# Kernel tuning notes

Hardware: AMD Instinct MI355X
Metric: run time of the kernel (lower is better)

The kernel has to match this reference:

```python
import jax, jax.numpy as jnp
import numpy as np

B, S, D = 2, 2048, 2048
H = 32
HD = D // H  # 64


def setup_inputs() -> dict:
    key = jax.random.key(0)
    ks = jax.random.split(key, 7)
    s = 1.0 / np.sqrt(D)
    return {
        "hidden_states": jax.random.normal(ks[0], (B, S, D), dtype=jnp.float32),
        "Wq": jax.random.normal(ks[1], (D, D), dtype=jnp.float32) * s,
        "Wk": jax.random.normal(ks[2], (D, D), dtype=jnp.float32) * s,
        "Wv": jax.random.normal(ks[3], (D, D), dtype=jnp.float32) * s,
        "Wf": jax.random.normal(ks[4], (H, D), dtype=jnp.float32) * s,
        "bf": jax.random.normal(ks[5], (H,), dtype=jnp.float32) * 0.1,
        "Wo": jax.random.normal(ks[6], (D, D), dtype=jnp.float32) * s,
    }


def _forgetting_attn(x, Wq, Wk, Wv, Wf, bf, Wo):
    b, s, _ = x.shape
    # projections (torch Linear: y = x @ W.T)
    q = (x @ Wq.T).reshape(b, s, H, HD)
    k = (x @ Wk.T).reshape(b, s, H, HD)
    v = (x @ Wv.T).reshape(b, s, H, HD)
    # per-head log-sigmoid forget gates, fp32, cumulative sum over time
    f = jax.nn.log_sigmoid((x @ Wf.T + bf).astype(jnp.float32))  # [b, s, H]
    c = jnp.cumsum(f, axis=1)  # [b, s, H]
    scale = 1.0 / np.sqrt(HD)
    # scores with forget bias: c_i - c_j
    scores = jnp.einsum("bihd,bjhd->bhij", q, k) * scale
    scores = scores + (c[:, :, None, :] - c[:, None, :, :]).transpose(0, 3, 1, 2)
    causal = jnp.tril(jnp.ones((s, s), dtype=bool))
    scores = jnp.where(causal[None, None], scores, -jnp.inf)
    p = jax.nn.softmax(scores, axis=-1)
    o = jnp.einsum("bhij,bjhd->bihd", p, v).reshape(b, s, D)
    return o @ Wo.T


def reference(hidden_states, Wq, Wk, Wv, Wf, bf, Wo):
    return _forgetting_attn(hidden_states, Wq, Wk, Wv, Wf, bf, Wo)
```

## Files before the change

kernel.cpp:

```cpp
#include <hip/hip_runtime.h>
#include <math.h>

#define B 2
#define S 2048
#define D 2048
#define H 32
#define HD 64
#define M (B*S)

typedef short s16x8 __attribute__((ext_vector_type(8)));
typedef float f32x4 __attribute__((ext_vector_type(4)));

__device__ __forceinline__ unsigned short f2bf(float f) {
    unsigned u = __float_as_uint(f);
    return (unsigned short)((u + 0x7fffu + ((u >> 16) & 1u)) >> 16);
}
__device__ __forceinline__ float bf2f(unsigned short h) {
    return __uint_as_float(((unsigned)h) << 16);
}

__global__ __launch_bounds__(256) void split_kernel(
    const float* __restrict__ in, unsigned short* __restrict__ hi,
    unsigned short* __restrict__ lo, int n)
{
    const int idx = (blockIdx.x * 256 + threadIdx.x) * 8;
    if (idx >= n) return;
    float f[8];
    *(float4*)&f[0] = *(const float4*)(in + idx);
    *(float4*)&f[4] = *(const float4*)(in + idx + 4);
    unsigned short h[8], l[8];
    #pragma unroll
    for (int e = 0; e < 8; ++e) {
        h[e] = f2bf(f[e]);
        l[e] = f2bf(f[e] - bf2f(h[e]));
    }
    *(s16x8*)&hi[idx] = *(s16x8*)&h[0];
    *(s16x8*)&lo[idx] = *(s16x8*)&l[0];
}

#define GBM 128
#define GBN 128
#define GBK 32
#define GLD (GBK + 8)

__global__ __launch_bounds__(256) void gemm_pre(
    const unsigned short* __restrict__ Agh, const unsigned short* __restrict__ Agl,
    const unsigned short* __restrict__ Bgh, const unsigned short* __restrict__ Bgl,
    float* __restrict__ Cf, unsigned short* __restrict__ Ch,
    unsigned short* __restrict__ Cl, int Ndim, int Kdim)
{
    __shared__ unsigned short Ah[GBM * GLD], Al[GBM * GLD];
    __shared__ unsigned short Bh[GBN * GLD], Bl[GBN * GLD];
    const int tid = threadIdx.x;
    const int nwg = gridDim.x, cpx = nwg >> 3;
    const int wg = (blockIdx.x & 7) * cpx + (blockIdx.x >> 3);
    const int ntn = Ndim / GBN;
    const int m0 = (wg / ntn) * GBM, n0 = (wg % ntn) * GBN;

    const int row = tid >> 1;
    const int seg = (tid & 1) << 4;
    const size_t abase = (size_t)(m0 + row) * Kdim + seg;
    const size_t bbase = (size_t)(n0 + row) * Kdim + seg;
    const int sbase = row * GLD + seg;

    const int wv = tid >> 6, lane = tid & 63;
    const int wr = (wv >> 1) << 6, wc = (wv & 1) << 6;
    const int fr = lane & 15, ko = (lane >> 4) << 3;

    f32x4 acc[4][4] = {};
    for (int k0 = 0; k0 < Kdim; k0 += GBK) {
        *(s16x8*)&Ah[sbase]     = *(const s16x8*)&Agh[abase + k0];
        *(s16x8*)&Ah[sbase + 8] = *(const s16x8*)&Agh[abase + k0 + 8];
        *(s16x8*)&Al[sbase]     = *(const s16x8*)&Agl[abase + k0];
        *(s16x8*)&Al[sbase + 8] = *(const s16x8*)&Agl[abase + k0 + 8];
        *(s16x8*)&Bh[sbase]     = *(const s16x8*)&Bgh[bbase + k0];
        *(s16x8*)&Bh[sbase + 8] = *(const s16x8*)&Bgh[bbase + k0 + 8];
        *(s16x8*)&Bl[sbase]     = *(const s16x8*)&Bgl[bbase + k0];
        *(s16x8*)&Bl[sbase + 8] = *(const s16x8*)&Bgl[bbase + k0 + 8];
        __syncthreads();
        s16x8 fah[4], fal[4], fbh[4], fbl[4];
        #pragma unroll
        for (int m = 0; m < 4; ++m) {
            const int r = (wr + m * 16 + fr) * GLD + ko;
            fah[m] = *(s16x8*)&Ah[r];
            fal[m] = *(s16x8*)&Al[r];
        }
        #pragma unroll
        for (int n = 0; n < 4; ++n) {
            const int r = (wc + n * 16 + fr) * GLD + ko;
            fbh[n] = *(s16x8*)&Bh[r];
            fbl[n] = *(s16x8*)&Bl[r];
        }
        #pragma unroll
        for (int m = 0; m < 4; ++m)
            #pragma unroll
            for (int n = 0; n < 4; ++n) {
                acc[m][n] = __builtin_amdgcn_mfma_f32_16x16x32_bf16(fah[m], fbh[n], acc[m][n], 0, 0, 0);
                acc[m][n] = __builtin_amdgcn_mfma_f32_16x16x32_bf16(fah[m], fbl[n], acc[m][n], 0, 0, 0);
                acc[m][n] = __builtin_amdgcn_mfma_f32_16x16x32_bf16(fal[m], fbh[n], acc[m][n], 0, 0, 0);
            }
        __syncthreads();
    }
    const int crow0 = m0 + wr + ((lane >> 4) << 2);
    const int ccol0 = n0 + wc + fr;
    #pragma unroll
    for (int m = 0; m < 4; ++m)
        #pragma unroll
        for (int n = 0; n < 4; ++n)
            #pragma unroll
            for (int r = 0; r < 4; ++r) {
                const float c = acc[m][n][r];
                const size_t idx = (size_t)(crow0 + m * 16 + r) * Ndim + ccol0 + n * 16;
                if (Cf) Cf[idx] = c;
                if (Ch) {
                    const unsigned short hh = f2bf(c);
                    Ch[idx] = hh;
                    if (Cl) Cl[idx] = f2bf(c - bf2f(hh));
                }
            }
}

__global__ __launch_bounds__(256) void fgate_kernel(
    const float* __restrict__ x, const float* __restrict__ Wf,
    const float* __restrict__ bfv, float* __restrict__ F)
{
    __shared__ float xs[D];
    const int bs = blockIdx.x;
    const float* xr = x + (size_t)bs * D;
    for (int i = threadIdx.x * 4; i < D; i += 256 * 4)
        *(float4*)&xs[i] = *(const float4*)&xr[i];
    __syncthreads();
    const int wave = threadIdx.x >> 6, lane = threadIdx.x & 63;
    for (int h = wave * 8; h < wave * 8 + 8; ++h) {
        const float* wr = Wf + (size_t)h * D;
        float sum = 0.f;
        for (int i = lane * 4; i < D; i += 64 * 4) {
            float4 w4 = *(const float4*)&wr[i];
            sum += xs[i]*w4.x + xs[i+1]*w4.y + xs[i+2]*w4.z + xs[i+3]*w4.w;
        }
        #pragma unroll
        for (int off = 32; off > 0; off >>= 1) sum += __shfl_down(sum, off);
        if (lane == 0) {
            float z = sum + bfv[h];
            F[(size_t)bs * H + h] = fminf(z, 0.f) - log1pf(expf(-fabsf(z)));
        }
    }
}

__global__ __launch_bounds__(256) void cumsum_kernel(float* __restrict__ F)
{
    const int b = blockIdx.x >> 5;
    const int h = blockIdx.x & 31;
    float* base = F + (size_t)b * S * H + h;
    __shared__ float part[256];
    const int t = threadIdx.x;
    float v[8];
    float run = 0.f;
    #pragma unroll
    for (int i = 0; i < 8; ++i) {
        v[i] = base[(size_t)(t * 8 + i) * H];
        run += v[i];
        v[i] = run;
    }
    part[t] = run;
    __syncthreads();
    for (int off = 1; off < 256; off <<= 1) {
        float add = (t >= off) ? part[t - off] : 0.f;
        __syncthreads();
        part[t] += add;
        __syncthreads();
    }
    const float offs = (t > 0) ? part[t - 1] : 0.f;
    #pragma unroll
    for (int i = 0; i < 8; ++i)
        base[(size_t)(t * 8 + i) * H] = v[i] + offs;
}

#define QBLK 128
#define KV 64
#define PLD 72
#define SCALE 0.125f

__global__ __launch_bounds__(256, 4) void attn_mfma2(
    const unsigned short* __restrict__ Qh, const unsigned short* __restrict__ Ql,
    const unsigned short* __restrict__ Kh, const unsigned short* __restrict__ Vh,
    const float* __restrict__ C,
    unsigned short* __restrict__ Oh, unsigned short* __restrict__ Ol)
{
    __shared__ unsigned short Ks[KV * PLD];
    __shared__ unsigned short Vt[HD * PLD];
    __shared__ unsigned short Pb[4 * 32 * PLD];
    __shared__ float cj[KV];

    const int qt = (int)gridDim.x - 1 - blockIdx.x;
    const int b = blockIdx.z >> 5, h = blockIdx.z & 31;
    const int q0 = qt * QBLK;
    const int tid = threadIdx.x, wv = tid >> 6, lane = tid & 63;
    const int g = lane >> 4, fr = lane & 15;

    s16x8 qfh[2][2], qfl[2][2];
    {
        const size_t qb = (size_t)(b * S + q0 + wv * 32) * D + h * HD;
        #pragma unroll
        for (int m = 0; m < 2; ++m)
            #pragma unroll
            for (int kd = 0; kd < 2; ++kd) {
                const size_t off = qb + (size_t)(m * 16 + fr) * D + kd * 32 + g * 8;
                qfh[m][kd] = *(const s16x8*)&Qh[off];
                qfl[m][kd] = *(const s16x8*)&Ql[off];
            }
    }

    f32x4 Oa[2][4] = {};
    float mr[2][4], lr[2][4];
    #pragma unroll
    for (int m = 0; m < 2; ++m)
        #pragma unroll
        for (int r = 0; r < 4; ++r) { mr[m][r] = -INFINITY; lr[m][r] = 0.f; }

    const int imax = q0 + wv * 32 + 31;
    const int nj = (q0 + QBLK) / KV;
    unsigned short* Pw = &Pb[wv * 32 * PLD];

    for (int jt = 0; jt < nj; ++jt) {
        const int j0 = jt * KV;
        {
            const int row = tid >> 2;
            const int seg = (tid & 3) << 4;
            const size_t goff = (size_t)(b * S + j0 + row) * D + h * HD + seg;
            *(s16x8*)&Ks[row * PLD + seg]     = *(const s16x8*)&Kh[goff];
            *(s16x8*)&Ks[row * PLD + seg + 8] = *(const s16x8*)&Kh[goff + 8];
            s16x8 v0 = *(const s16x8*)&Vh[goff];
            s16x8 v1 = *(const s16x8*)&Vh[goff + 8];
            #pragma unroll
            for (int e = 0; e < 8; ++e) {
                Vt[(seg + e) * PLD + row]     = (unsigned short)v0[e];
                Vt[(seg + 8 + e) * PLD + row] = (unsigned short)v1[e];
            }
            if (tid < KV)
                cj[tid] = C[(size_t)(b * S + j0 + tid) * H + h];
        }
        __syncthreads();

        if (j0 <= imax) {
            s16x8 kfr[4][2];
            #pragma unroll
            for (int n = 0; n < 4; ++n)
                #pragma unroll
                for (int kd = 0; kd < 2; ++kd)
                    kfr[n][kd] = *(s16x8*)&Ks[(n * 16 + fr) * PLD + kd * 32 + g * 8];
            f32x4 sa[2][4] = {};
            #pragma unroll
            for (int m = 0; m < 2; ++m)
                #pragma unroll
                for (int n = 0; n < 4; ++n) {
                    #pragma unroll
                    for (int kd = 0; kd < 2; ++kd) {
                        sa[m][n] = __builtin_amdgcn_mfma_f32_16x16x32_bf16(qfh[m][kd], kfr[n][kd], sa[m][n], 0, 0, 0);
                        sa[m][n] = __builtin_amdgcn_mfma_f32_16x16x32_bf16(qfl[m][kd], kfr[n][kd], sa[m][n], 0, 0, 0);
                    }
                }
            float cjr[4];
            #pragma unroll
            for (int n = 0; n < 4; ++n) cjr[n] = cj[fr + 16 * n];
            float sc[2][4][4];
            float tm[2][4];
            #pragma unroll
            for (int m = 0; m < 2; ++m)
                #pragma unroll
                for (int r = 0; r < 4; ++r) tm[m][r] = -INFINITY;
            #pragma unroll
            for (int m = 0; m < 2; ++m)
                #pragma unroll
                for (int n = 0; n < 4; ++n)
                    #pragma unroll
                    for (int r = 0; r < 4; ++r) {
                        const int qrow = q0 + wv * 32 + m * 16 + g * 4 + r;
                        const int jcol = j0 + fr + 16 * n;
                        float s = sa[m][n][r] * SCALE - cjr[n];
                        s = (jcol <= qrow) ? s : -INFINITY;
                        sc[m][n][r] = s;
                        tm[m][r] = fmaxf(tm[m][r], s);
                    }
            #pragma unroll
            for (int m = 0; m < 2; ++m)
                #pragma unroll
                for (int r = 0; r < 4; ++r) {
                    float v = tm[m][r];
                    v = fmaxf(v, __shfl_xor(v, 1));
                    v = fmaxf(v, __shfl_xor(v, 2));
                    v = fmaxf(v, __shfl_xor(v, 4));
                    v = fmaxf(v, __shfl_xor(v, 8));
                    tm[m][r] = v;
                }
            #pragma unroll
            for (int m = 0; m < 2; ++m)
                #pragma unroll
                for (int r = 0; r < 4; ++r) {
                    const float newm = fmaxf(mr[m][r], tm[m][r]);
                    const float corr = __expf(mr[m][r] - newm);
                    mr[m][r] = newm;
                    lr[m][r] *= corr;
                    #pragma unroll
                    for (int n = 0; n < 4; ++n) Oa[m][n][r] *= corr;
                }
            #pragma unroll
            for (int m = 0; m < 2; ++m) {
                float ps[4];
                #pragma unroll
                for (int r = 0; r < 4; ++r) ps[r] = 0.f;
                #pragma unroll
                for (int n = 0; n < 4; ++n)
                    #pragma unroll
                    for (int r = 0; r < 4; ++r) {
                        const float p = __expf(sc[m][n][r] - mr[m][r]);
                        ps[r] += p;
                        Pw[(m * 16 + g * 4 + r) * PLD + fr + 16 * n] = f2bf(p);
                    }
                #pragma unroll
                for (int r = 0; r < 4; ++r) {
                    float v = ps[r];
                    v += __shfl_xor(v, 1);
                    v += __shfl_xor(v, 2);
                    v += __shfl_xor(v, 4);
                    v += __shfl_xor(v, 8);
                    lr[m][r] += v;
                }
            }
            s16x8 pf[2][2], vfr[4][2];
            #pragma unroll
            for (int m = 0; m < 2; ++m)
                #pragma unroll
                for (int kj = 0; kj < 2; ++kj)
                    pf[m][kj] = *(s16x8*)&Pw[(fr + 16 * m) * PLD + kj * 32 + g * 8];
            #pragma unroll
            for (int n = 0; n < 4; ++n)
                #pragma unroll
                for (int kj = 0; kj < 2; ++kj)
                    vfr[n][kj] = *(s16x8*)&Vt[(n * 16 + fr) * PLD + kj * 32 + g * 8];
            #pragma unroll
            for (int m = 0; m < 2; ++m)
                #pragma unroll
                for (int n = 0; n < 4; ++n)
                    #pragma unroll
                    for (int kj = 0; kj < 2; ++kj)
                        Oa[m][n] = __builtin_amdgcn_mfma_f32_16x16x32_bf16(pf[m][kj], vfr[n][kj], Oa[m][n], 0, 0, 0);
        }
        __syncthreads();
    }

    #pragma unroll
    for (int m = 0; m < 2; ++m)
        #pragma unroll
        for (int r = 0; r < 4; ++r) {
            const float inv = 1.f / lr[m][r];
            const size_t rowb = (size_t)(b * S + q0 + wv * 32 + m * 16 + g * 4 + r) * D + h * HD;
            #pragma unroll
            for (int n = 0; n < 4; ++n) {
                const float c = Oa[m][n][r] * inv;
                const unsigned short hh = f2bf(c);
                Oh[rowb + fr + 16 * n] = hh;
                Ol[rowb + fr + 16 * n] = f2bf(c - bf2f(hh));
            }
        }
}

extern "C" void kernel_launch(void* const* d_in, const int* in_sizes, int n_in,
                              void* d_out, int out_size, void* d_ws, size_t ws_size,
                              hipStream_t stream) {
    const float* x  = (const float*)d_in[0];
    const float* Wq = (const float*)d_in[1];
    const float* Wk = (const float*)d_in[2];
    const float* Wv = (const float*)d_in[3];
    const float* Wf = (const float*)d_in[4];
    const float* bf = (const float*)d_in[5];
    const float* Wo = (const float*)d_in[6];
    float* out = (float*)d_out;

    const size_t MD = (size_t)M * D, DD = (size_t)D * D;
    unsigned short* Xh = (unsigned short*)d_ws;
    unsigned short* Xl = Xh + MD;
    unsigned short* Wh = Xl + MD;
    unsigned short* Wl = Wh + DD;
    unsigned short* Qh = Wl + DD;
    unsigned short* Ql = Qh + MD;
    unsigned short* Kh = Ql + MD;
    unsigned short* Vh = Kh + MD;
    float* Fc = (float*)(Vh + MD);
    unsigned short* Oh = Xh;
    unsigned short* Ol = Xl;

    const dim3 blk(256);
    const dim3 ggrid((M / GBM) * (D / GBN));
    const int nMD = (int)MD, nDD = (int)DD;
    const dim3 gsx(nMD / 8 / 256), gsw(nDD / 8 / 256);

    split_kernel<<<gsx, blk, 0, stream>>>(x, Xh, Xl, nMD);
    split_kernel<<<gsw, blk, 0, stream>>>(Wq, Wh, Wl, nDD);
    gemm_pre<<<ggrid, blk, 0, stream>>>(Xh, Xl, Wh, Wl, nullptr, Qh, Ql, D, D);
    split_kernel<<<gsw, blk, 0, stream>>>(Wk, Wh, Wl, nDD);
    gemm_pre<<<ggrid, blk, 0, stream>>>(Xh, Xl, Wh, Wl, nullptr, Kh, nullptr, D, D);
    split_kernel<<<gsw, blk, 0, stream>>>(Wv, Wh, Wl, nDD);
    gemm_pre<<<ggrid, blk, 0, stream>>>(Xh, Xl, Wh, Wl, nullptr, Vh, nullptr, D, D);
    fgate_kernel<<<dim3(M), blk, 0, stream>>>(x, Wf, bf, Fc);
    cumsum_kernel<<<dim3(B * H), blk, 0, stream>>>(Fc);
    attn_mfma2<<<dim3(S / QBLK, 1, B * H), blk, 0, stream>>>(Qh, Ql, Kh, Vh, Fc, Oh, Ol);
    split_kernel<<<gsw, blk, 0, stream>>>(Wo, Wh, Wl, nDD);
    gemm_pre<<<ggrid, blk, 0, stream>>>(Oh, Ol, Wh, Wl, out, nullptr, nullptr, D, D);
}
```

Measured before the change: 982.3 us.

## Enlarge attention query tile to 8 waves, transpose cumsum, stage output stores

The attention kernel now uses 256-row query blocks with 512 threads (8 waves), so each K/V tile loaded into shared memory serves twice as many queries and global K/V traffic drops. The P buffer is shrunk to 16 rows per wave and P·V is issued per m-slice, and the cumsum output is written head-major so gate values load contiguously. Output is staged through shared memory for 16-byte coalesced stores. The risks are fewer blocks (lower occupancy, coarser causal load balance), and the unchanged qfh/Oa indexing with wv*32 must still be consistent with the new wave count.

```diff
diff --git a/kernel.cpp b/kernel.cpp
--- a/kernel.cpp
+++ b/kernel.cpp
@@ -147,11 +147,13 @@
     }
 }
 
-__global__ __launch_bounds__(256) void cumsum_kernel(float* __restrict__ F)
+__global__ __launch_bounds__(256) void cumsum_kernel(
+    const float* __restrict__ F, float* __restrict__ Ct)
 {
     const int b = blockIdx.x >> 5;
     const int h = blockIdx.x & 31;
-    float* base = F + (size_t)b * S * H + h;
+    const float* base = F + (size_t)b * S * H + h;
+    float* outb = Ct + (size_t)(b * H + h) * S;
     __shared__ float part[256];
     const int t = threadIdx.x;
     float v[8];
@@ -173,23 +175,24 @@
     const float offs = (t > 0) ? part[t - 1] : 0.f;
     #pragma unroll
     for (int i = 0; i < 8; ++i)
-        base[(size_t)(t * 8 + i) * H] = v[i] + offs;
-}
-
-#define QBLK 128
+        outb[t * 8 + i] = v[i] + offs;
+}
+
+#define QBLK 256
+#define NW 8
 #define KV 64
 #define PLD 72
 #define SCALE 0.125f
 
-__global__ __launch_bounds__(256, 4) void attn_mfma2(
+__global__ __launch_bounds__(512) void attn_mfma3(
     const unsigned short* __restrict__ Qh, const unsigned short* __restrict__ Ql,
     const unsigned short* __restrict__ Kh, const unsigned short* __restrict__ Vh,
-    const float* __restrict__ C,
+    const float* __restrict__ Ct,
     unsigned short* __restrict__ Oh, unsigned short* __restrict__ Ol)
 {
     __shared__ unsigned short Ks[KV * PLD];
     __shared__ unsigned short Vt[HD * PLD];
-    __shared__ unsigned short Pb[4 * 32 * PLD];
+    __shared__ unsigned short Pb[NW * 16 * PLD];
     __shared__ float cj[KV];
 
     const int qt = (int)gridDim.x - 1 - blockIdx.x;
@@ -220,25 +223,21 @@
 
     const int imax = q0 + wv * 32 + 31;
     const int nj = (q0 + QBLK) / KV;
-    unsigned short* Pw = &Pb[wv * 32 * PLD];
+    unsigned short* Pw = &Pb[wv * 16 * PLD];
 
     for (int jt = 0; jt < nj; ++jt) {
         const int j0 = jt * KV;
         {
-            const int row = tid >> 2;
-            const int seg = (tid & 3) << 4;
+            const int row = tid >> 3;
+            const int seg = (tid & 7) << 3;
             const size_t goff = (size_t)(b * S + j0 + row) * D + h * HD + seg;
-            *(s16x8*)&Ks[row * PLD + seg]     = *(const s16x8*)&Kh[goff];
-            *(s16x8*)&Ks[row * PLD + seg + 8] = *(const s16x8*)&Kh[goff + 8];
+            *(s16x8*)&Ks[row * PLD + seg] = *(const s16x8*)&Kh[goff];
             s16x8 v0 = *(const s16x8*)&Vh[goff];
-            s16x8 v1 = *(const s16x8*)&Vh[goff + 8];
-            #pragma unroll
-            for (int e = 0; e < 8; ++e) {
-                Vt[(seg + e) * PLD + row]     = (unsigned short)v0[e];
-                Vt[(seg + 8 + e) * PLD + row] = (unsigned short)v1[e];
-            }
+            #pragma unroll
+            for (int e = 0; e < 8; ++e)
+                Vt[(seg + e) * PLD + row] = (unsigned short)v0[e];
             if (tid < KV)
-                cj[tid] = C[(size_t)(b * S + j0 + tid) * H + h];
+                cj[tid] = Ct[(size_t)(b * H + h) * S + j0 + tid];
         }
         __syncthreads();
 
@@ -304,6 +303,12 @@
                     #pragma unroll
                     for (int n = 0; n < 4; ++n) Oa[m][n][r] *= corr;
                 }
+            s16x8 vfr[4][2];
+            #pragma unroll
+            for (int n = 0; n < 4; ++n)
+                #pragma unroll
+                for (int kj = 0; kj < 2; ++kj)
+                    vfr[n][kj] = *(s16x8*)&Vt[(n * 16 + fr) * PLD + kj * 32 + g * 8];
             #pragma unroll
             for (int m = 0; m < 2; ++m) {
                 float ps[4];
@@ -315,7 +320,7 @@
                     for (int r = 0; r < 4; ++r) {
                         const float p = __expf(sc[m][n][r] - mr[m][r]);
                         ps[r] += p;
-                        Pw[(m * 16 + g * 4 + r) * PLD + fr + 16 * n] = f2bf(p);
+                        Pw[(g * 4 + r) * PLD + fr + 16 * n] = f2bf(p);
                     }
                 #pragma unroll
                 for (int r = 0; r < 4; ++r) {
@@ -326,43 +331,45 @@
                     v += __shfl_xor(v, 8);
                     lr[m][r] += v;
                 }
-            }
-            s16x8 pf[2][2], vfr[4][2];
-            #pragma unroll
-            for (int m = 0; m < 2; ++m)
+                s16x8 pf[2];
                 #pragma unroll
                 for (int kj = 0; kj < 2; ++kj)
-                    pf[m][kj] = *(s16x8*)&Pw[(fr + 16 * m) * PLD + kj * 32 + g * 8];
-            #pragma unroll
-            for (int n = 0; n < 4; ++n)
-                #pragma unroll
-                for (int kj = 0; kj < 2; ++kj)
-                    vfr[n][kj] = *(s16x8*)&Vt[(n * 16 + fr) * PLD + kj * 32 + g * 8];
-            #pragma unroll
-            for (int m = 0; m < 2; ++m)
+                    pf[kj] = *(s16x8*)&Pw[fr * PLD + kj * 32 + g * 8];
                 #pragma unroll
                 for (int n = 0; n < 4; ++n)
                     #pragma unroll
                     for (int kj = 0; kj < 2; ++kj)
-                        Oa[m][n] = __builtin_amdgcn_mfma_f32_16x16x32_bf16(pf[m][kj], vfr[n][kj], Oa[m][n], 0, 0, 0);
-        }
-        __syncthreads();
-    }
-
-    #pragma unroll
-    for (int m = 0; m < 2; ++m)
-        #pragma unroll
-        for (int r = 0; r < 4; ++r) {
-            const float inv = 1.f / lr[m][r];
-            const size_t rowb = (size_t)(b * S + q0 + wv * 32 + m * 16 + g * 4 + r) * D + h * HD;
-            #pragma unroll
-            for (int n = 0; n < 4; ++n) {
-                const float c = Oa[m][n][r] * inv;
-                const unsigned short hh = f2bf(c);
-                Oh[rowb + fr + 16 * n] = hh;
-                Ol[rowb + fr + 16 * n] = f2bf(c - bf2f(hh));
+                        Oa[m][n] = __builtin_amdgcn_mfma_f32_16x16x32_bf16(pf[kj], vfr[n][kj], Oa[m][n], 0, 0, 0);
             }
         }
+        __syncthreads();
+    }
+
+    #pragma unroll
+    for (int m = 0; m < 2; ++m) {
+        float inv[4];
+        #pragma unroll
+        for (int r = 0; r < 4; ++r) inv[r] = 1.f / lr[m][r];
+        const int row_l = lane >> 2;
+        const int ch = (lane & 3) << 4;
+        const size_t grow = (size_t)(b * S + q0 + wv * 32 + m * 16 + row_l) * D + h * HD + ch;
+        #pragma unroll
+        for (int n = 0; n < 4; ++n)
+            #pragma unroll
+            for (int r = 0; r < 4; ++r)
+                Pw[(g * 4 + r) * PLD + fr + 16 * n] = f2bf(Oa[m][n][r] * inv[r]);
+        *(s16x8*)&Oh[grow]     = *(s16x8*)&Pw[row_l * PLD + ch];
+        *(s16x8*)&Oh[grow + 8] = *(s16x8*)&Pw[row_l * PLD + ch + 8];
+        #pragma unroll
+        for (int n = 0; n < 4; ++n)
+            #pragma unroll
+            for (int r = 0; r < 4; ++r) {
+                const float c = Oa[m][n][r] * inv[r];
+                Pw[(g * 4 + r) * PLD + fr + 16 * n] = f2bf(c - bf2f(f2bf(c)));
+            }
+        *(s16x8*)&Ol[grow]     = *(s16x8*)&Pw[row_l * PLD + ch];
+        *(s16x8*)&Ol[grow + 8] = *(s16x8*)&Pw[row_l * PLD + ch + 8];
+    }
 }
 
 extern "C" void kernel_launch(void* const* d_in, const int* in_sizes, int n_in,
@@ -387,6 +394,7 @@
     unsigned short* Kh = Ql + MD;
     unsigned short* Vh = Kh + MD;
     float* Fc = (float*)(Vh + MD);
+    float* Ct = Fc + (size_t)M * H;
     unsigned short* Oh = Xh;
     unsigned short* Ol = Xl;
 
@@ -403,8 +411,8 @@
     split_kernel<<<gsw, blk, 0, stream>>>(Wv, Wh, Wl, nDD);
     gemm_pre<<<ggrid, blk, 0, stream>>>(Xh, Xl, Wh, Wl, nullptr, Vh, nullptr, D, D);
     fgate_kernel<<<dim3(M), blk, 0, stream>>>(x, Wf, bf, Fc);
-    cumsum_kernel<<<dim3(B * H), blk, 0, stream>>>(Fc);
-    attn_mfma2<<<dim3(S / QBLK, 1, B * H), blk, 0, stream>>>(Qh, Ql, Kh, Vh, Fc, Oh, Ol);
+    cumsum_kernel<<<dim3(B * H), blk, 0, stream>>>(Fc, Ct);
+    attn_mfma3<<<dim3(S / QBLK, 1, B * H), dim3(512), 0, stream>>>(Qh, Ql, Kh, Vh, Ct, Oh, Ol);
     split_kernel<<<gsw, blk, 0, stream>>>(Wo, Wh, Wl, nDD);
     gemm_pre<<<ggrid, blk, 0, stream>>>(Oh, Ol, Wh, Wl, out, nullptr, nullptr, D, D);
 }
```

Result: faster. 898.3 us (-8.6%).
